# Kernel optimization log

Hardware: AMD Instinct MI355X
Metric: run time of the kernel (lower is better)

The kernel has to match this reference:

```python
import jax, jax.numpy as jnp
import numpy as np

B, S, D_IN, D_HID, D_OUT = 32, 512, 768, 3072, 768


def setup_inputs() -> dict:
    key = jax.random.key(0)
    k1, k2, k3, k4 = jax.random.split(key, 4)
    init_k = float(np.sqrt(1.0 / D_IN))
    init_k2 = float(np.sqrt(1.0 / D_HID))
    x = jax.random.normal(k1, (B, S, D_IN), dtype=jnp.float32)
    in_weight = jax.random.uniform(k2, (D_HID, D_IN), dtype=jnp.float32, minval=-init_k, maxval=init_k)
    in_bias = jax.random.uniform(k3, (D_HID,), dtype=jnp.float32, minval=-init_k, maxval=init_k)
    out_weight = jax.random.uniform(k4, (D_HID, D_OUT), dtype=jnp.float32, minval=-init_k2, maxval=init_k2)
    return {"x": x, "in_weight": in_weight, "in_bias": in_bias, "out_weight": out_weight}


def reference(x, in_weight, in_bias, out_weight):
    # flatten leading dims to tokens: [B*S, D_IN]
    lead = x.shape[:-1]
    xt = x.reshape(-1, in_weight.shape[1])
    # hidden = GELU(x @ W_in^T + b)   (in_weight stored [hidden, in])
    h = jax.nn.gelu(jnp.einsum('td,hd->th', xt, in_weight) + in_bias, approximate=False)
    # out = hidden @ W_out            (out_weight stored [hidden, out]; no output bias)
    out = jnp.einsum('th,ho->to', h, out_weight)
    return out.reshape(*lead, out_weight.shape[1])
```

## Files before the change

kernel.cpp:

```cpp
#include <hip/hip_runtime.h>

typedef short bf16x8 __attribute__((ext_vector_type(8)));
typedef float f32x4  __attribute__((ext_vector_type(4)));

__device__ __forceinline__ unsigned short f2bf(float f) {
    unsigned int u = __float_as_uint(f);
    u += 0x7FFFu + ((u >> 16) & 1u);
    return (unsigned short)(u >> 16);
}

__device__ __forceinline__ float gelu_f(float x) {
    float x2 = x * x;
    float u = x * (-1.5957691216f - 0.0713548162f * x2);
    float e = __expf(u);
    return x * __builtin_amdgcn_rcpf(1.0f + e);
}

__global__ void cvt_f32_bf16(const float* __restrict__ in,
                             unsigned short* __restrict__ out, int n4) {
    int stride = gridDim.x * blockDim.x;
    for (int i = blockIdx.x * blockDim.x + threadIdx.x; i < n4; i += stride) {
        float4 v = ((const float4*)in)[i];
        ushort4 r;
        r.x = f2bf(v.x); r.y = f2bf(v.y); r.z = f2bf(v.z); r.w = f2bf(v.w);
        ((ushort4*)out)[i] = r;
    }
}

__global__ void transpose_cvt(const float* __restrict__ in,
                              unsigned short* __restrict__ out, int H, int O) {
    __shared__ float tile[32][33];
    int o0 = blockIdx.x * 32, h0 = blockIdx.y * 32;
    int tx = threadIdx.x, ty = threadIdx.y;
    #pragma unroll
    for (int r = 0; r < 32; r += 8)
        tile[ty + r][tx] = in[(size_t)(h0 + ty + r) * O + o0 + tx];
    __syncthreads();
    #pragma unroll
    for (int r = 0; r < 32; r += 8) {
        int o = ty + r;
        out[(size_t)(o0 + o) * H + h0 + tx] = f2bf(tile[tx][o]);
    }
}

template <int K, int N>
__global__ __launch_bounds__(512, 2) void gemm1_8ph(
    const unsigned short* __restrict__ A,
    const unsigned short* __restrict__ B,
    const float* __restrict__ bias,
    unsigned short* __restrict__ C) {
    __shared__ __align__(16) char lds[131072];
    const int t = threadIdx.x;
    const int w = t >> 6, l = t & 63;
    constexpr int ntiles = N >> 8;

    int bid = blockIdx.x, nwg = gridDim.x;
    int wgid = ((nwg & 7) == 0) ? ((bid & 7) * (nwg >> 3) + (bid >> 3)) : bid;
    const int mt = wgid / ntiles, nt = wgid % ntiles;
    const int m0 = mt << 8, n0 = nt << 8;
    const int wr = w >> 2, wc = w & 3;

    const int u1 = t + 512;
    const int gu0 = (t >> 2) * K + (((t & 3) ^ ((t >> 3) & 3)) << 3);
    const int gu1 = (u1 >> 2) * K + (((u1 & 3) ^ ((u1 >> 3) & 3)) << 3);
    const unsigned short* Abase = A + (size_t)m0 * K;
    const unsigned short* Bbase = B + (size_t)n0 * K;

#define STAGE(PTR, KT, KS, REG) { \
    const unsigned short* g_ = (PTR) + (KT) * 64 + (KS) * 32; \
    __builtin_amdgcn_global_load_lds( \
        (const __attribute__((address_space(1))) void*)(g_ + gu0), \
        (__attribute__((address_space(3))) void*)(lds + (REG) + t * 16), 16, 0, 0); \
    __builtin_amdgcn_global_load_lds( \
        (const __attribute__((address_space(1))) void*)(g_ + gu1), \
        (__attribute__((address_space(3))) void*)(lds + (REG) + 8192 + t * 16), 16, 0, 0); }
#define PIN() { __builtin_amdgcn_sched_barrier(0); asm volatile("" ::: "memory"); }
#define GATE() { asm volatile("s_waitcnt vmcnt(8)\n\ts_barrier" ::: "memory"); \
                 __builtin_amdgcn_sched_barrier(0); }
#define LGKM() { __builtin_amdgcn_sched_barrier(0); \
                 asm volatile("s_waitcnt lgkmcnt(0)" ::: "memory"); \
                 __builtin_amdgcn_sched_barrier(0); }
#define RDB(RG) { const char* p_ = lds + (RG) + boffb; \
    bv[0] = *(const bf16x8*)(p_);        bv[1] = *(const bf16x8*)(p_ + 1024); \
    bv[2] = *(const bf16x8*)(p_ + 2048); bv[3] = *(const bf16x8*)(p_ + 3072); }
#define RDA(RG, MH) { const char* p_ = lds + (RG) + aoffb + (MH) * 4096; \
    av[0] = *(const bf16x8*)(p_);        av[1] = *(const bf16x8*)(p_ + 1024); \
    av[2] = *(const bf16x8*)(p_ + 2048); av[3] = *(const bf16x8*)(p_ + 3072); }
#define MFMA16(MB) \
    _Pragma("unroll") \
    for (int mi = 0; mi < 4; ++mi) { \
        _Pragma("unroll") \
        for (int ni = 0; ni < 4; ++ni) \
            acc[MB * 4 + mi][ni] = __builtin_amdgcn_mfma_f32_16x16x32_bf16( \
                av[mi], bv[ni], acc[MB * 4 + mi][ni], 0, 0, 0); \
    } \
    __builtin_amdgcn_s_setprio(0); \
    __builtin_amdgcn_sched_barrier(0);

    const int cR = l >> 4, lr = l & 15;
    const int swz = (cR ^ ((lr >> 1) & 3)) << 4;
    const int aoffb = (wr * 128 + lr) * 64 + swz;
    const int boffb = 32768 + (wc * 64 + lr) * 64 + swz;

    f32x4 acc[8][4];
    {
        f32x4 z = {0.f, 0.f, 0.f, 0.f};
        #pragma unroll
        for (int i = 0; i < 8; ++i)
            #pragma unroll
            for (int j = 0; j < 4; ++j) acc[i][j] = z;
    }
    bf16x8 av[4], bv[4];

    constexpr int NTK = K >> 6;
    constexpr int NT2 = K >> 7;

    STAGE(Abase, 0, 0, 0);             PIN();
    STAGE(Bbase, 0, 0, 32768);         PIN();
    STAGE(Abase, 0, 1, 16384);         PIN();
    STAGE(Bbase, 0, 1, 49152);         PIN();
    STAGE(Abase, 1, 0, 65536);         PIN();
    STAGE(Bbase, 1, 0, 98304);         PIN();

    for (int tt = 0; tt < NT2; ++tt) {
        const int k1 = (2 * tt + 1 < NTK) ? 2 * tt + 1 : NTK - 1;
        const int k2 = (2 * tt + 2 < NTK) ? 2 * tt + 2 : NTK - 1;
        const int k3 = (2 * tt + 3 < NTK) ? 2 * tt + 3 : NTK - 1;
        GATE(); RDB(0); RDA(0, 0);
        STAGE(Abase, k1, 1, 81920);
        LGKM(); __builtin_amdgcn_s_setprio(1); MFMA16(0);
        RDA(0, 1);
        STAGE(Bbase, k1, 1, 114688);
        LGKM(); __builtin_amdgcn_s_setprio(1); MFMA16(1);
        GATE(); RDB(16384); RDA(16384, 0);
        STAGE(Abase, k2, 0, 0);
        LGKM(); __builtin_amdgcn_s_setprio(1); MFMA16(0);
        RDA(16384, 1);
        STAGE(Bbase, k2, 0, 32768);
        LGKM(); __builtin_amdgcn_s_setprio(1); MFMA16(1);
        GATE(); RDB(65536); RDA(65536, 0);
        STAGE(Abase, k2, 1, 16384);
        LGKM(); __builtin_amdgcn_s_setprio(1); MFMA16(0);
        RDA(65536, 1);
        STAGE(Bbase, k2, 1, 49152);
        LGKM(); __builtin_amdgcn_s_setprio(1); MFMA16(1);
        GATE(); RDB(81920); RDA(81920, 0);
        STAGE(Abase, k3, 0, 65536);
        LGKM(); __builtin_amdgcn_s_setprio(1); MFMA16(0);
        RDA(81920, 1);
        STAGE(Bbase, k3, 0, 98304);
        LGKM(); __builtin_amdgcn_s_setprio(1); MFMA16(1);
    }
#undef STAGE
#undef PIN
#undef GATE
#undef LGKM
#undef RDB
#undef RDA
#undef MFMA16

    const int colb = n0 + wc * 64 + lr;
    float bvs[4];
    #pragma unroll
    for (int ni = 0; ni < 4; ++ni) bvs[ni] = bias[colb + ni * 16];
    #pragma unroll
    for (int mi = 0; mi < 8; ++mi)
        #pragma unroll
        for (int j = 0; j < 4; ++j) {
            size_t row = m0 + wr * 128 + mi * 16 + cR * 4 + j;
            #pragma unroll
            for (int ni = 0; ni < 4; ++ni) {
                float v = acc[mi][ni][j] + bvs[ni];
                C[row * N + colb + ni * 16] = f2bf(gelu_f(v));
            }
        }
}

template <int EPI, int K, int N>
__global__ __launch_bounds__(512, 2) void gemm_k2(
    const unsigned short* __restrict__ A,
    const unsigned short* __restrict__ B,
    const float* __restrict__ bias,
    void* __restrict__ Cp) {
    constexpr int BN = 192, NREP = 3;
    constexpr int BHALF = 32768;
    constexpr int LBUF  = BHALF + BN * 128;
    __shared__ __align__(16) char lds[2 * LBUF];
    const int t = threadIdx.x;
    const int w = t >> 6, l = t & 63;
    constexpr int ntiles = N / BN;

    int bid = blockIdx.x;
    int nwg = gridDim.x;
    int wgid = ((nwg & 7) == 0) ? ((bid & 7) * (nwg >> 3) + (bid >> 3)) : bid;
    const int mt = wgid / ntiles, nt = wgid % ntiles;
    const int m0 = mt << 8, n0 = nt * BN;
    const int wr = w >> 2, wc = w & 3;

    const int rA = t >> 3;
    const int sl = (t & 7) ^ (rA & 7);

    auto stage = [&](int kt, char* dst) {
        const int kc = kt * 64 + sl * 8;
        #pragma unroll
        for (int i = 0; i < 4; ++i) {
            const unsigned short* ga = A + (size_t)(m0 + i * 64 + rA) * K + kc;
            char* la = dst + i * 8192 + (w << 10);
            __builtin_amdgcn_global_load_lds((const __attribute__((address_space(1))) void*)ga,
                                             (__attribute__((address_space(3))) void*)la, 16, 0, 0);
        }
        #pragma unroll
        for (int i = 0; i < NREP; ++i) {
            const unsigned short* gb = B + (size_t)(n0 + i * 64 + rA) * K + kc;
            char* lb = dst + BHALF + i * 8192 + (w << 10);
            __builtin_amdgcn_global_load_lds((const __attribute__((address_space(1))) void*)gb,
                                             (__attribute__((address_space(3))) void*)lb, 16, 0, 0);
        }
    };

    const int swz = ((l >> 4) ^ (l & 7)) << 4;
    const int aoff0 = (wr * 128 + (l & 15)) * 128 + swz;
    const int aoffX = aoff0 ^ 64;
    const int boff0 = BHALF + (wc * (BN / 4) + (l & 15)) * 128 + swz;
    const int boffX = boff0 ^ 64;

    f32x4 acc[8][NREP];
    {
        f32x4 z = {0.f, 0.f, 0.f, 0.f};
        #pragma unroll
        for (int i = 0; i < 8; ++i)
            #pragma unroll
            for (int j = 0; j < NREP; ++j) acc[i][j] = z;
    }

    constexpr int NT = K >> 6;
    stage(0, lds);
    __builtin_amdgcn_sched_barrier(0);
    asm volatile("" ::: "memory");
    stage(1, lds + LBUF);

    for (int kt = 0; kt < NT; ++kt) {
        asm volatile("s_waitcnt vmcnt(7)\n\ts_barrier" ::: "memory");
        __builtin_amdgcn_sched_barrier(0);
        const char* base = lds + (kt & 1) * LBUF;
        bf16x8 av[4][2], bv[NREP][2];
        #pragma unroll
        for (int ni = 0; ni < NREP; ++ni) {
            bv[ni][0] = *(const bf16x8*)(base + boff0 + ni * 2048);
            bv[ni][1] = *(const bf16x8*)(base + boffX + ni * 2048);
        }
        #pragma unroll
        for (int mi = 0; mi < 4; ++mi) {
            av[mi][0] = *(const bf16x8*)(base + aoff0 + mi * 2048);
            av[mi][1] = *(const bf16x8*)(base + aoffX + mi * 2048);
        }
        #pragma unroll
        for (int ksel = 0; ksel < 2; ++ksel)
            #pragma unroll
            for (int mi = 0; mi < 4; ++mi)
                #pragma unroll
                for (int ni = 0; ni < NREP; ++ni)
                    acc[mi][ni] = __builtin_amdgcn_mfma_f32_16x16x32_bf16(
                        av[mi][ksel], bv[ni][ksel], acc[mi][ni], 0, 0, 0);
        #pragma unroll
        for (int mi = 0; mi < 4; ++mi) {
            av[mi][0] = *(const bf16x8*)(base + aoff0 + (4 + mi) * 2048);
            av[mi][1] = *(const bf16x8*)(base + aoffX + (4 + mi) * 2048);
        }
        #pragma unroll
        for (int ksel = 0; ksel < 2; ++ksel)
            #pragma unroll
            for (int mi = 0; mi < 4; ++mi)
                #pragma unroll
                for (int ni = 0; ni < NREP; ++ni)
                    acc[4 + mi][ni] = __builtin_amdgcn_mfma_f32_16x16x32_bf16(
                        av[mi][ksel], bv[ni][ksel], acc[4 + mi][ni], 0, 0, 0);
        __builtin_amdgcn_sched_barrier(0);
        asm volatile("s_waitcnt lgkmcnt(0)\n\ts_barrier" ::: "memory");
        __builtin_amdgcn_sched_barrier(0);
        stage(kt + 2 < NT ? kt + 2 : NT - 1, lds + (kt & 1) * LBUF);
    }

    if constexpr (EPI == 0) {
        unsigned short* Cb = (unsigned short*)Cp;
        #pragma unroll
        for (int ni = 0; ni < NREP; ++ni) {
            int col = n0 + wc * (BN / 4) + ni * 16 + (l & 15);
            float bvs = bias[col];
            #pragma unroll
            for (int mi = 0; mi < 8; ++mi) {
                int rbase = m0 + wr * 128 + mi * 16 + ((l >> 4) << 2);
                #pragma unroll
                for (int j = 0; j < 4; ++j) {
                    float v = acc[mi][ni][j] + bvs;
                    Cb[(size_t)(rbase + j) * N + col] = f2bf(gelu_f(v));
                }
            }
        }
    } else {
        float* Cf = (float*)Cp;
        #pragma unroll
        for (int ni = 0; ni < NREP; ++ni) {
            int col = n0 + wc * (BN / 4) + ni * 16 + (l & 15);
            #pragma unroll
            for (int mi = 0; mi < 8; ++mi) {
                int rbase = m0 + wr * 128 + mi * 16 + ((l >> 4) << 2);
                #pragma unroll
                for (int j = 0; j < 4; ++j)
                    Cf[(size_t)(rbase + j) * N + col] = acc[mi][ni][j];
            }
        }
    }
}

extern "C" void kernel_launch(void* const* d_in, const int* in_sizes, int n_in,
                              void* d_out, int out_size, void* d_ws, size_t ws_size,
                              hipStream_t stream) {
    const float* x  = (const float*)d_in[0];
    const float* w1 = (const float*)d_in[1];
    const float* b1 = (const float*)d_in[2];
    const float* w2 = (const float*)d_in[3];
    float* out = (float*)d_out;

    const int T = 16384, DIN = 768, DH = 3072, DOUT = 768;

    unsigned short* xb  = (unsigned short*)d_ws;
    unsigned short* w1b = xb  + (size_t)T * DIN;
    unsigned short* w2t = w1b + (size_t)DH * DIN;
    unsigned short* h   = w2t + (size_t)DOUT * DH;

    size_t fixed = ((size_t)T * DIN + (size_t)DH * DIN + (size_t)DOUT * DH) * 2;
    int CH = T;
    while (CH > 256 && fixed + (size_t)CH * DH * 2 > ws_size) CH >>= 1;

    cvt_f32_bf16<<<2048, 256, 0, stream>>>(x, xb, T * DIN / 4);
    cvt_f32_bf16<<<1024, 256, 0, stream>>>(w1, w1b, DH * DIN / 4);
    transpose_cvt<<<dim3(DOUT / 32, DH / 32), dim3(32, 8), 0, stream>>>(w2, w2t, DH, DOUT);

    for (int c0 = 0; c0 < T; c0 += CH) {
        gemm1_8ph<768, 3072><<<(CH / 256) * (DH / 256), 512, 0, stream>>>(
            xb + (size_t)c0 * DIN, w1b, b1, h);
        gemm_k2<1, 3072, 768><<<(CH / 256) * (DOUT / 192), 512, 0, stream>>>(
            h, w2t, b1, out + (size_t)c0 * DOUT);
    }
}
```

Before: 196.8 us.

## Generalize 8-phase pipelined GEMM and use it for the second projection

```diff
diff --git a/kernel.cpp b/kernel.cpp
--- a/kernel.cpp
+++ b/kernel.cpp
@@ -43,21 +43,22 @@
     }
 }
 
-template <int K, int N>
-__global__ __launch_bounds__(512, 2) void gemm1_8ph(
+template <int EPI, int K, int N, int BN>
+__global__ __launch_bounds__(512, 2) void gemm_8ph(
     const unsigned short* __restrict__ A,
     const unsigned short* __restrict__ B,
     const float* __restrict__ bias,
-    unsigned short* __restrict__ C) {
+    void* __restrict__ Cp) {
+    constexpr int NREP = BN / 64;
     __shared__ __align__(16) char lds[131072];
     const int t = threadIdx.x;
     const int w = t >> 6, l = t & 63;
-    constexpr int ntiles = N >> 8;
+    constexpr int ntiles = N / BN;
 
     int bid = blockIdx.x, nwg = gridDim.x;
     int wgid = ((nwg & 7) == 0) ? ((bid & 7) * (nwg >> 3) + (bid >> 3)) : bid;
     const int mt = wgid / ntiles, nt = wgid % ntiles;
-    const int m0 = mt << 8, n0 = nt << 8;
+    const int m0 = mt << 8, n0 = nt * BN;
     const int wr = w >> 2, wc = w & 3;
 
     const int u1 = t + 512;
@@ -81,16 +82,16 @@
                  asm volatile("s_waitcnt lgkmcnt(0)" ::: "memory"); \
                  __builtin_amdgcn_sched_barrier(0); }
 #define RDB(RG) { const char* p_ = lds + (RG) + boffb; \
-    bv[0] = *(const bf16x8*)(p_);        bv[1] = *(const bf16x8*)(p_ + 1024); \
-    bv[2] = *(const bf16x8*)(p_ + 2048); bv[3] = *(const bf16x8*)(p_ + 3072); }
+    _Pragma("unroll") \
+    for (int ni_ = 0; ni_ < NREP; ++ni_) bv[ni_] = *(const bf16x8*)(p_ + ni_ * 1024); }
 #define RDA(RG, MH) { const char* p_ = lds + (RG) + aoffb + (MH) * 4096; \
     av[0] = *(const bf16x8*)(p_);        av[1] = *(const bf16x8*)(p_ + 1024); \
     av[2] = *(const bf16x8*)(p_ + 2048); av[3] = *(const bf16x8*)(p_ + 3072); }
-#define MFMA16(MB) \
+#define MFMAQ(MB) \
     _Pragma("unroll") \
     for (int mi = 0; mi < 4; ++mi) { \
         _Pragma("unroll") \
-        for (int ni = 0; ni < 4; ++ni) \
+        for (int ni = 0; ni < NREP; ++ni) \
             acc[MB * 4 + mi][ni] = __builtin_amdgcn_mfma_f32_16x16x32_bf16( \
                 av[mi], bv[ni], acc[MB * 4 + mi][ni], 0, 0, 0); \
     } \
@@ -100,17 +101,17 @@
     const int cR = l >> 4, lr = l & 15;
     const int swz = (cR ^ ((lr >> 1) & 3)) << 4;
     const int aoffb = (wr * 128 + lr) * 64 + swz;
-    const int boffb = 32768 + (wc * 64 + lr) * 64 + swz;
-
-    f32x4 acc[8][4];
+    const int boffb = 32768 + (wc * (BN / 4) + lr) * 64 + swz;
+
+    f32x4 acc[8][NREP];
     {
         f32x4 z = {0.f, 0.f, 0.f, 0.f};
         #pragma unroll
         for (int i = 0; i < 8; ++i)
             #pragma unroll
-            for (int j = 0; j < 4; ++j) acc[i][j] = z;
-    }
-    bf16x8 av[4], bv[4];
+            for (int j = 0; j < NREP; ++j) acc[i][j] = z;
+    }
+    bf16x8 av[4], bv[NREP];
 
     constexpr int NTK = K >> 6;
     constexpr int NT2 = K >> 7;
@@ -128,28 +129,28 @@
         const int k3 = (2 * tt + 3 < NTK) ? 2 * tt + 3 : NTK - 1;
         GATE(); RDB(0); RDA(0, 0);
         STAGE(Abase, k1, 1, 81920);
-        LGKM(); __builtin_amdgcn_s_setprio(1); MFMA16(0);
+        LGKM(); __builtin_amdgcn_s_setprio(1); MFMAQ(0);
         RDA(0, 1);
         STAGE(Bbase, k1, 1, 114688);
-        LGKM(); __builtin_amdgcn_s_setprio(1); MFMA16(1);
+        LGKM(); __builtin_amdgcn_s_setprio(1); MFMAQ(1);
         GATE(); RDB(16384); RDA(16384, 0);
         STAGE(Abase, k2, 0, 0);
-        LGKM(); __builtin_amdgcn_s_setprio(1); MFMA16(0);
+        LGKM(); __builtin_amdgcn_s_setprio(1); MFMAQ(0);
         RDA(16384, 1);
         STAGE(Bbase, k2, 0, 32768);
-        LGKM(); __builtin_amdgcn_s_setprio(1); MFMA16(1);
+        LGKM(); __builtin_amdgcn_s_setprio(1); MFMAQ(1);
         GATE(); RDB(65536); RDA(65536, 0);
         STAGE(Abase, k2, 1, 16384);
-        LGKM(); __builtin_amdgcn_s_setprio(1); MFMA16(0);
+        LGKM(); __builtin_amdgcn_s_setprio(1); MFMAQ(0);
         RDA(65536, 1);
         STAGE(Bbase, k2, 1, 49152);
-        LGKM(); __builtin_amdgcn_s_setprio(1); MFMA16(1);
+        LGKM(); __builtin_amdgcn_s_setprio(1); MFMAQ(1);
         GATE(); RDB(81920); RDA(81920, 0);
         STAGE(Abase, k3, 0, 65536);
-        LGKM(); __builtin_amdgcn_s_setprio(1); MFMA16(0);
+        LGKM(); __builtin_amdgcn_s_setprio(1); MFMAQ(0);
         RDA(81920, 1);
         STAGE(Bbase, k3, 0, 98304);
-        LGKM(); __builtin_amdgcn_s_setprio(1); MFMA16(1);
+        LGKM(); __builtin_amdgcn_s_setprio(1); MFMAQ(1);
     }
 #undef STAGE
 #undef PIN
@@ -157,159 +158,36 @@
 #undef LGKM
 #undef RDB
 #undef RDA
-#undef MFMA16
-
-    const int colb = n0 + wc * 64 + lr;
-    float bvs[4];
-    #pragma unroll
-    for (int ni = 0; ni < 4; ++ni) bvs[ni] = bias[colb + ni * 16];
-    #pragma unroll
-    for (int mi = 0; mi < 8; ++mi)
-        #pragma unroll
-        for (int j = 0; j < 4; ++j) {
-            size_t row = m0 + wr * 128 + mi * 16 + cR * 4 + j;
+#undef MFMAQ
+
+    const int colb = n0 + wc * (BN / 4) + lr;
+    if constexpr (EPI == 0) {
+        unsigned short* Cb = (unsigned short*)Cp;
+        float bvs[NREP];
+        #pragma unroll
+        for (int ni = 0; ni < NREP; ++ni) bvs[ni] = bias[colb + ni * 16];
+        #pragma unroll
+        for (int mi = 0; mi < 8; ++mi)
             #pragma unroll
-            for (int ni = 0; ni < 4; ++ni) {
-                float v = acc[mi][ni][j] + bvs[ni];
-                C[row * N + colb + ni * 16] = f2bf(gelu_f(v));
+            for (int j = 0; j < 4; ++j) {
+                size_t row = m0 + wr * 128 + mi * 16 + cR * 4 + j;
+                #pragma unroll
+                for (int ni = 0; ni < NREP; ++ni) {
+                    float v = acc[mi][ni][j] + bvs[ni];
+                    Cb[row * N + colb + ni * 16] = f2bf(gelu_f(v));
+                }
             }
-        }
-}
-
-template <int EPI, int K, int N>
-__global__ __launch_bounds__(512, 2) void gemm_k2(
-    const unsigned short* __restrict__ A,
-    const unsigned short* __restrict__ B,
-    const float* __restrict__ bias,
-    void* __restrict__ Cp) {
-    constexpr int BN = 192, NREP = 3;
-    constexpr int BHALF = 32768;
-    constexpr int LBUF  = BHALF + BN * 128;
-    __shared__ __align__(16) char lds[2 * LBUF];
-    const int t = threadIdx.x;
-    const int w = t >> 6, l = t & 63;
-    constexpr int ntiles = N / BN;
-
-    int bid = blockIdx.x;
-    int nwg = gridDim.x;
-    int wgid = ((nwg & 7) == 0) ? ((bid & 7) * (nwg >> 3) + (bid >> 3)) : bid;
-    const int mt = wgid / ntiles, nt = wgid % ntiles;
-    const int m0 = mt << 8, n0 = nt * BN;
-    const int wr = w >> 2, wc = w & 3;
-
-    const int rA = t >> 3;
-    const int sl = (t & 7) ^ (rA & 7);
-
-    auto stage = [&](int kt, char* dst) {
-        const int kc = kt * 64 + sl * 8;
-        #pragma unroll
-        for (int i = 0; i < 4; ++i) {
-            const unsigned short* ga = A + (size_t)(m0 + i * 64 + rA) * K + kc;
-            char* la = dst + i * 8192 + (w << 10);
-            __builtin_amdgcn_global_load_lds((const __attribute__((address_space(1))) void*)ga,
-                                             (__attribute__((address_space(3))) void*)la, 16, 0, 0);
-        }
-        #pragma unroll
-        for (int i = 0; i < NREP; ++i) {
-            const unsigned short* gb = B + (size_t)(n0 + i * 64 + rA) * K + kc;
-            char* lb = dst + BHALF + i * 8192 + (w << 10);
-            __builtin_amdgcn_global_load_lds((const __attribute__((address_space(1))) void*)gb,
-                                             (__attribute__((address_space(3))) void*)lb, 16, 0, 0);
-        }
-    };
-
-    const int swz = ((l >> 4) ^ (l & 7)) << 4;
-    const int aoff0 = (wr * 128 + (l & 15)) * 128 + swz;
-    const int aoffX = aoff0 ^ 64;
-    const int boff0 = BHALF + (wc * (BN / 4) + (l & 15)) * 128 + swz;
-    const int boffX = boff0 ^ 64;
-
-    f32x4 acc[8][NREP];
-    {
-        f32x4 z = {0.f, 0.f, 0.f, 0.f};
-        #pragma unroll
-        for (int i = 0; i < 8; ++i)
+    } else {
+        float* Cf = (float*)Cp;
+        #pragma unroll
+        for (int mi = 0; mi < 8; ++mi)
             #pragma unroll
-            for (int j = 0; j < NREP; ++j) acc[i][j] = z;
-    }
-
-    constexpr int NT = K >> 6;
-    stage(0, lds);
-    __builtin_amdgcn_sched_barrier(0);
-    asm volatile("" ::: "memory");
-    stage(1, lds + LBUF);
-
-    for (int kt = 0; kt < NT; ++kt) {
-        asm volatile("s_waitcnt vmcnt(7)\n\ts_barrier" ::: "memory");
-        __builtin_amdgcn_sched_barrier(0);
-        const char* base = lds + (kt & 1) * LBUF;
-        bf16x8 av[4][2], bv[NREP][2];
-        #pragma unroll
-        for (int ni = 0; ni < NREP; ++ni) {
-            bv[ni][0] = *(const bf16x8*)(base + boff0 + ni * 2048);
-            bv[ni][1] = *(const bf16x8*)(base + boffX + ni * 2048);
-        }
-        #pragma unroll
-        for (int mi = 0; mi < 4; ++mi) {
-            av[mi][0] = *(const bf16x8*)(base + aoff0 + mi * 2048);
-            av[mi][1] = *(const bf16x8*)(base + aoffX + mi * 2048);
-        }
-        #pragma unroll
-        for (int ksel = 0; ksel < 2; ++ksel)
-            #pragma unroll
-            for (int mi = 0; mi < 4; ++mi)
+            for (int j = 0; j < 4; ++j) {
+                size_t row = m0 + wr * 128 + mi * 16 + cR * 4 + j;
                 #pragma unroll
                 for (int ni = 0; ni < NREP; ++ni)
-                    acc[mi][ni] = __builtin_amdgcn_mfma_f32_16x16x32_bf16(
-                        av[mi][ksel], bv[ni][ksel], acc[mi][ni], 0, 0, 0);
-        #pragma unroll
-        for (int mi = 0; mi < 4; ++mi) {
-            av[mi][0] = *(const bf16x8*)(base + aoff0 + (4 + mi) * 2048);
-            av[mi][1] = *(const bf16x8*)(base + aoffX + (4 + mi) * 2048);
-        }
-        #pragma unroll
-        for (int ksel = 0; ksel < 2; ++ksel)
-            #pragma unroll
-            for (int mi = 0; mi < 4; ++mi)
-                #pragma unroll
-                for (int ni = 0; ni < NREP; ++ni)
-                    acc[4 + mi][ni] = __builtin_amdgcn_mfma_f32_16x16x32_bf16(
-                        av[mi][ksel], bv[ni][ksel], acc[4 + mi][ni], 0, 0, 0);
-        __builtin_amdgcn_sched_barrier(0);
-        asm volatile("s_waitcnt lgkmcnt(0)\n\ts_barrier" ::: "memory");
-        __builtin_amdgcn_sched_barrier(0);
-        stage(kt + 2 < NT ? kt + 2 : NT - 1, lds + (kt & 1) * LBUF);
-    }
-
-    if constexpr (EPI == 0) {
-        unsigned short* Cb = (unsigned short*)Cp;
-        #pragma unroll
-        for (int ni = 0; ni < NREP; ++ni) {
-            int col = n0 + wc * (BN / 4) + ni * 16 + (l & 15);
-            float bvs = bias[col];
-            #pragma unroll
-            for (int mi = 0; mi < 8; ++mi) {
-                int rbase = m0 + wr * 128 + mi * 16 + ((l >> 4) << 2);
-                #pragma unroll
-                for (int j = 0; j < 4; ++j) {
-                    float v = acc[mi][ni][j] + bvs;
-                    Cb[(size_t)(rbase + j) * N + col] = f2bf(gelu_f(v));
-                }
+                    Cf[row * N + colb + ni * 16] = acc[mi][ni][j];
             }
-        }
-    } else {
-        float* Cf = (float*)Cp;
-        #pragma unroll
-        for (int ni = 0; ni < NREP; ++ni) {
-            int col = n0 + wc * (BN / 4) + ni * 16 + (l & 15);
-            #pragma unroll
-            for (int mi = 0; mi < 8; ++mi) {
-                int rbase = m0 + wr * 128 + mi * 16 + ((l >> 4) << 2);
-                #pragma unroll
-                for (int j = 0; j < 4; ++j)
-                    Cf[(size_t)(rbase + j) * N + col] = acc[mi][ni][j];
-            }
-        }
     }
 }
 
@@ -338,9 +216,9 @@
     transpose_cvt<<<dim3(DOUT / 32, DH / 32), dim3(32, 8), 0, stream>>>(w2, w2t, DH, DOUT);
 
     for (int c0 = 0; c0 < T; c0 += CH) {
-        gemm1_8ph<768, 3072><<<(CH / 256) * (DH / 256), 512, 0, stream>>>(
+        gemm_8ph<0, 768, 3072, 256><<<(CH / 256) * (DH / 256), 512, 0, stream>>>(
             xb + (size_t)c0 * DIN, w1b, b1, h);
-        gemm_k2<1, 3072, 768><<<(CH / 256) * (DOUT / 192), 512, 0, stream>>>(
+        gemm_8ph<1, 3072, 768, 192><<<(CH / 256) * (DOUT / 192), 512, 0, stream>>>(
             h, w2t, b1, out + (size_t)c0 * DOUT);
     }
 }
```

Result: faster. 188.0 us (-4.5%).
